# Performance work log

Measured on AMD Instinct MI355X. Metric: run time of the kernel, lower is better.

The kernel has to match this reference:

```python
import jax, jax.numpy as jnp
import numpy as np
from jax import lax

L, CB, D, K = 4, 256, 512, 3   # layers, bottleneck, dconv_size, kernel
B, T = 16, 4096                # batch, frames
EPS = 1e-5


def _binarize(w):
    # bitwise weight quantization: sign(w), straight-through in bwd
    return w + lax.stop_gradient(jnp.sign(w) - w)


def _conv1d(x, w, b, dilation=1, groups=1, pad=(0, 0)):
    # x: [N, C, T], w: [O, I/groups, K]
    y = lax.conv_general_dilated(
        x, w, window_strides=(1,), padding=[pad], rhs_dilation=(dilation,),
        dimension_numbers=("NCH", "OIH", "NCH"), feature_group_count=groups)
    return y + b[None, :, None]


def _prelu(x, a):
    return jnp.where(x >= 0, x, a * x)


def _bn(x, g, b):
    # training-mode BatchNorm1d over (batch, time) per channel
    mean = jnp.mean(x, axis=(0, 2), keepdims=True)
    var = jnp.var(x, axis=(0, 2), keepdims=True)
    xn = (x - mean) * lax.rsqrt(var + EPS)
    return xn * g[None, :, None] + b[None, :, None]


def setup_inputs() -> dict:
    key = jax.random.key(0)
    ks = jax.random.split(key, 8)
    s = 0.05
    return {
        "x":   jax.random.normal(ks[0], (B, CB, T), jnp.float32),
        "w1":  jax.random.normal(ks[1], (L, D, CB, 1), jnp.float32) * s,
        "b1":  jnp.zeros((L, D), jnp.float32),
        "a1":  jnp.full((L,), 0.25, jnp.float32),
        "g1":  jnp.ones((L, D), jnp.float32),
        "be1": jnp.zeros((L, D), jnp.float32),
        "wd":  jax.random.normal(ks[2], (L, D, 1, K), jnp.float32) * s,
        "bd":  jnp.zeros((L, D), jnp.float32),
        "a2":  jnp.full((L,), 0.25, jnp.float32),
        "g2":  jnp.ones((L, D), jnp.float32),
        "be2": jnp.zeros((L, D), jnp.float32),
        "w2":  jax.random.normal(ks[3], (L, CB, D, 1), jnp.float32) * s,
        "b2":  jnp.zeros((L, CB), jnp.float32),
    }


def reference(x, w1, b1, a1, g1, be1, wd, bd, a2, g2, be2, w2, b2):
    resid = x
    for i in range(L):
        dil = 2 ** i
        pad_left = dil * (K - 1)  # causal/chomped padding keeps length T
        x = _conv1d(x, _binarize(w1[i]), b1[i])                       # 1x1: CB->D
        x = _bn(_prelu(x, a1[i]), g1[i], be1[i])
        x = _conv1d(x, _binarize(wd[i]), bd[i], dilation=dil,
                    groups=D, pad=(pad_left, 0))                       # depthwise dilated
        x = _bn(_prelu(x, a2[i]), g2[i], be2[i])
        x = _conv1d(x, _binarize(w2[i]), b2[i])                       # 1x1: D->CB
    return x + resid
```

## Files before the change

kernel.cpp:

```cpp
#include <hip/hip_runtime.h>
#include <stdint.h>
#include <stddef.h>

#define NL   4
#define CBC  256
#define DCH  512
#define KW   3
#define BATCH 16
#define TT   4096
#define BT   (BATCH*TT)
#define EPSB 1e-5f

typedef __bf16 bf16_t;
typedef __attribute__((ext_vector_type(8))) __bf16 bf16x8;
typedef __attribute__((ext_vector_type(4))) float f32x4;
typedef __attribute__((ext_vector_type(8))) unsigned short us8;
typedef __attribute__((ext_vector_type(4))) unsigned short us4;

static __device__ __forceinline__ unsigned short f2bf(float f) {
    union { float f; uint32_t u; } v; v.f = f;
    uint32_t u = v.u;
    u += 0x7FFFu + ((u >> 16) & 1u);
    return (unsigned short)(u >> 16);
}
static __device__ __forceinline__ float bf2f(unsigned short b) {
    union { uint32_t u; float f; } v; v.u = ((uint32_t)b) << 16;
    return v.f;
}
static __device__ __forceinline__ bf16x8 as_bf16x8(us8 u) {
    return __builtin_bit_cast(bf16x8, u);
}
static __device__ __forceinline__ float signf_(float w) {
    return (w > 0.f) ? 1.f : ((w < 0.f) ? -1.f : 0.f);
}

typedef __attribute__((address_space(1))) void as1_void;
typedef __attribute__((address_space(3))) void as3_void;
static __device__ __forceinline__ void gload_lds16(const unsigned short* g, unsigned short* l) {
    __builtin_amdgcn_global_load_lds((as1_void*)g, (as3_void*)l, 16, 0, 0);
}

__global__ void prep_kernel(const float* __restrict__ w1, const float* __restrict__ wd,
                            unsigned short* __restrict__ W1S, float* __restrict__ WDS) {
    const int NW1 = NL * DCH * CBC;
    const int NWD = NL * DCH * KW;
    int idx = blockIdx.x * 256 + threadIdx.x;
    if (idx < NW1) {
        W1S[idx] = f2bf(signf_(w1[idx]));
    } else if (idx < NW1 + NWD) {
        int j = idx - NW1;
        WDS[j] = signf_(wd[j]);
    }
}

__global__ void transpose_in(const float* __restrict__ x, unsigned short* __restrict__ XA) {
    __shared__ unsigned short tile[64][72];
    const int t0 = blockIdx.x * 64, c0 = blockIdx.y * 64, b = blockIdx.z;
    const int tid = threadIdx.x;
    {
        const int cl = tid >> 2;
        const int tl = (tid & 3) * 16;
        const float* src = x + ((size_t)(b * CBC + c0 + cl)) * TT + t0 + tl;
        #pragma unroll
        for (int u = 0; u < 16; u += 4) {
            float4 f = *(const float4*)(src + u);
            tile[cl][tl + u + 0] = f2bf(f.x);
            tile[cl][tl + u + 1] = f2bf(f.y);
            tile[cl][tl + u + 2] = f2bf(f.z);
            tile[cl][tl + u + 3] = f2bf(f.w);
        }
    }
    __syncthreads();
    {
        const int tr = tid >> 2;
        const int cc = (tid & 3) * 16;
        us8 o0, o1;
        #pragma unroll
        for (int e = 0; e < 8; ++e) { o0[e] = tile[cc + e][tr]; o1[e] = tile[cc + 8 + e][tr]; }
        unsigned short* dst = XA + ((size_t)(b * TT + t0 + tr)) * CBC + c0 + cc;
        *(us8*)dst = o0;
        *(us8*)(dst + 8) = o1;
    }
}

template<int K, int NMT, bool PRELU, bool FINAL, bool STATS>
__global__ __launch_bounds__(256, 4)
void gemm_kernel(const unsigned short* __restrict__ A,
                 const unsigned short* __restrict__ Bact,
                 const float* __restrict__ bias,
                 const float* __restrict__ aptr,
                 unsigned short* __restrict__ Obf,
                 float* __restrict__ Ofin,
                 const float* __restrict__ resid,
                 float* __restrict__ sums, float* __restrict__ sqs,
                 int M) {
    __shared__ union {
        unsigned short stage[2][4][2048];
        unsigned short sout[128 * 136];
    } sm;
    __shared__ float sstat[2][4][64];

    const int tid = threadIdx.x;

    const int nwg = NMT * (TT / 128) * BATCH;
    const int orig = blockIdx.x;
    const int logical = (orig & 7) * (nwg >> 3) + (orig >> 3);
    const int mt = logical % NMT;
    const int rest = logical / NMT;
    const int tt = rest & 31;
    const int bz = rest >> 5;
    const int t0 = tt * 128;
    const int m0 = mt * 128;
    const size_t n0 = (size_t)bz * TT + t0;

    const int lane = tid & 63;
    const int w    = tid >> 6;
    const int wm = w & 1, wn = w >> 1;
    const int l16 = lane & 15, q = lane >> 4;

    const int rS = tid >> 2;
    const int cS = ((tid & 3) ^ ((tid >> 3) & 3)) * 8;
    const unsigned short* gA0 = A + (size_t)(m0 + rS) * K + cS;
    const unsigned short* gA1 = A + (size_t)(m0 + 64 + rS) * K + cS;
    const unsigned short* gB0 = Bact + (n0 + rS) * K + cS;
    const unsigned short* gB1 = Bact + (n0 + 64 + rS) * K + cS;
    const int wofs = w << 9;

    auto STAGE = [&](int step, int buf) {
        const int k0 = step * 32;
        unsigned short* sb = &sm.stage[buf][0][0];
        gload_lds16(gA0 + k0, sb + 0 * 2048 + wofs);
        gload_lds16(gA1 + k0, sb + 1 * 2048 + wofs);
        gload_lds16(gB0 + k0, sb + 2 * 2048 + wofs);
        gload_lds16(gB1 + k0, sb + 3 * 2048 + wofs);
    };

    f32x4 acc[4][4];
    #pragma unroll
    for (int i = 0; i < 4; ++i)
        #pragma unroll
        for (int j = 0; j < 4; ++j)
            acc[i][j] = (f32x4){0.f, 0.f, 0.f, 0.f};

    const int csw = (q ^ ((l16 >> 1) & 3)) << 3;

    constexpr int NK = K / 32;
    STAGE(0, 0);
    asm volatile("s_waitcnt vmcnt(0)" ::: "memory");
    __builtin_amdgcn_s_barrier();
    __builtin_amdgcn_sched_barrier(0);

    #pragma unroll
    for (int k = 0; k < NK; ++k) {
        const int cur = k & 1;
        if (k + 1 < NK) STAGE(k + 1, cur ^ 1);
        const unsigned short* sb = &sm.stage[cur][0][0];
        bf16x8 af[4], bfv[4];
        #pragma unroll
        for (int i = 0; i < 4; ++i)
            af[i] = as_bf16x8(*(const us8*)(sb + wm * 2048 + (i * 16 + l16) * 32 + csw));
        #pragma unroll
        for (int j = 0; j < 4; ++j)
            bfv[j] = as_bf16x8(*(const us8*)(sb + (2 + wn) * 2048 + (j * 16 + l16) * 32 + csw));
        #pragma unroll
        for (int i = 0; i < 4; ++i)
            #pragma unroll
            for (int j = 0; j < 4; ++j)
                acc[i][j] = __builtin_amdgcn_mfma_f32_16x16x32_bf16(af[i], bfv[j], acc[i][j], 0, 0, 0);
        if (k + 1 < NK) {
            asm volatile("s_waitcnt vmcnt(0)" ::: "memory");
            __builtin_amdgcn_sched_barrier(0);
        }
        __builtin_amdgcn_s_barrier();
        __builtin_amdgcn_sched_barrier(0);
    }

    float alpha = 0.f;
    if constexpr (PRELU) alpha = aptr[0];

    if constexpr (FINAL) {
        #pragma unroll
        for (int i = 0; i < 4; ++i) {
            const int m_l = wm * 64 + i * 16 + q * 4;
            float bia[4];
            #pragma unroll
            for (int rg = 0; rg < 4; ++rg) bia[rg] = bias[m0 + m_l + rg];
            #pragma unroll
            for (int j = 0; j < 4; ++j) {
                const int n_l = wn * 64 + j * 16 + l16;
                const int t = t0 + n_l;
                #pragma unroll
                for (int rg = 0; rg < 4; ++rg) {
                    float v = acc[i][j][rg] + bia[rg];
                    size_t oidx = ((size_t)(bz * CBC + m0 + m_l + rg)) * TT + t;
                    Ofin[oidx] = v + resid[oidx];
                }
            }
        }
    } else {
        #pragma unroll
        for (int i = 0; i < 4; ++i) {
            const int m_l = wm * 64 + i * 16 + q * 4;
            float bia[4];
            #pragma unroll
            for (int rg = 0; rg < 4; ++rg) bia[rg] = bias[m0 + m_l + rg];
            #pragma unroll
            for (int j = 0; j < 4; ++j) {
                const int n_l = wn * 64 + j * 16 + l16;
                us4 pkv;
                #pragma unroll
                for (int rg = 0; rg < 4; ++rg) {
                    float v = acc[i][j][rg] + bia[rg];
                    if (PRELU) v = (v >= 0.f) ? v : alpha * v;
                    pkv[rg] = f2bf(v);
                }
                *(us4*)&sm.sout[n_l * 136 + m_l] = pkv;
            }
            if constexpr (STATS) {
                #pragma unroll
                for (int rg = 0; rg < 4; ++rg) {
                    float sv = 0.f, sq2 = 0.f;
                    #pragma unroll
                    for (int j = 0; j < 4; ++j) {
                        float v = acc[i][j][rg] + bia[rg];
                        if (PRELU) v = (v >= 0.f) ? v : alpha * v;
                        sv += v; sq2 += v * v;
                    }
                    #pragma unroll
                    for (int msk = 1; msk < 16; msk <<= 1) {
                        sv  += __shfl_xor(sv,  msk, 64);
                        sq2 += __shfl_xor(sq2, msk, 64);
                    }
                    if (l16 == 0) {
                        const int cl = i * 16 + q * 4 + rg;
                        sstat[0][w][cl] = sv;
                        sstat[1][w][cl] = sq2;
                    }
                }
            }
        }
        __syncthreads();
        const int rr = tid >> 4;
        const int c8 = (tid & 15) * 8;
        #pragma unroll
        for (int p = 0; p < 8; ++p) {
            const int n_l = p * 16 + rr;
            us8 v = *(const us8*)&sm.sout[n_l * 136 + c8];
            *(us8*)(Obf + (n0 + n_l) * M + m0 + c8) = v;
        }
        if constexpr (STATS) {
            if (tid < 128) {
                const int wmc = tid >> 6, cl = tid & 63;
                float S = sstat[0][wmc][cl] + sstat[0][wmc + 2][cl];
                float Q = sstat[1][wmc][cl] + sstat[1][wmc + 2][cl];
                atomicAdd(&sums[m0 + tid], S);
                atomicAdd(&sqs[m0 + tid], Q);
            }
        }
    }
}

__global__ __launch_bounds__(256)
void dwconv_kernel(const unsigned short* __restrict__ Y,
                   const float* __restrict__ sums1, const float* __restrict__ sqs1,
                   const float* __restrict__ g1, const float* __restrict__ be1,
                   const float* __restrict__ wds, const float* __restrict__ bd,
                   const float* __restrict__ a2p, int dil,
                   unsigned short* __restrict__ Z,
                   float* __restrict__ sums2, float* __restrict__ sqs2) {
    __shared__ float ssum[4][256];
    __shared__ float ssq[4][256];
    const int b = blockIdx.z;
    const int half = blockIdx.y;
    const int t0 = blockIdx.x * 64;
    const int tid = threadIdx.x;
    const int w = tid >> 6;
    const int lane = tid & 63;
    const int r = lane >> 5;
    const int cl = (lane & 31) * 8;
    const int c0 = half * 256 + cl;
    const float alpha = a2p[0];

    float s8[8], sh8[8], wv0[8], wv1[8], wv2[8], bb8[8];
    const float inv = 1.f / (float)BT;
    #pragma unroll
    for (int e = 0; e < 8; ++e) {
        const int d = c0 + e;
        float mean = sums1[d] * inv;
        float var = sqs1[d] * inv - mean * mean;
        float sc = g1[d] * rsqrtf(var + EPSB);
        s8[e] = sc;
        sh8[e] = be1[d] - mean * sc;
        wv0[e] = wds[d * 3 + 0]; wv1[e] = wds[d * 3 + 1]; wv2[e] = wds[d * 3 + 2];
        bb8[e] = bd[d];
    }

    float asum[8], asq[8];
    #pragma unroll
    for (int e = 0; e < 8; ++e) { asum[e] = 0.f; asq[e] = 0.f; }

    if (blockIdx.x == 0) {
        for (int it = 0; it < 8; ++it) {
            const int t = it * 8 + 2 * w + r;
            const size_t base = ((size_t)b * TT + t) * DCH + c0;
            float acc[8];
            {
                us8 y0 = *(const us8*)&Y[base];
                #pragma unroll
                for (int e = 0; e < 8; ++e)
                    acc[e] = wv2[e] * (s8[e] * bf2f(y0[e]) + sh8[e]) + bb8[e];
            }
            if (t >= dil) {
                us8 y1 = *(const us8*)&Y[base - (size_t)dil * DCH];
                #pragma unroll
                for (int e = 0; e < 8; ++e)
                    acc[e] += wv1[e] * (s8[e] * bf2f(y1[e]) + sh8[e]);
            }
            if (t >= 2 * dil) {
                us8 y2 = *(const us8*)&Y[base - (size_t)(2 * dil) * DCH];
                #pragma unroll
                for (int e = 0; e < 8; ++e)
                    acc[e] += wv0[e] * (s8[e] * bf2f(y2[e]) + sh8[e]);
            }
            us8 o;
            #pragma unroll
            for (int e = 0; e < 8; ++e) {
                float v = acc[e];
                v = (v >= 0.f) ? v : alpha * v;
                asum[e] += v; asq[e] += v * v;
                o[e] = f2bf(v);
            }
            *(us8*)&Z[base] = o;
        }
    } else {
        float W0s[8], W1s[8], W2s[8], shall[8];
        #pragma unroll
        for (int e = 0; e < 8; ++e) {
            W0s[e] = wv0[e] * s8[e];
            W1s[e] = wv1[e] * s8[e];
            W2s[e] = wv2[e] * s8[e];
            shall[e] = (wv0[e] + wv1[e] + wv2[e]) * sh8[e] + bb8[e];
        }
        const size_t d1 = (size_t)dil * DCH, d2 = 2 * d1;
        for (int it = 0; it < 8; ++it) {
            const int t = t0 + it * 8 + 2 * w + r;
            const size_t base = ((size_t)b * TT + t) * DCH + c0;
            us8 y0 = *(const us8*)&Y[base];
            us8 y1 = *(const us8*)&Y[base - d1];
            us8 y2 = *(const us8*)&Y[base - d2];
            us8 o;
            #pragma unroll
            for (int e = 0; e < 8; ++e) {
                float v = W2s[e] * bf2f(y0[e]) + W1s[e] * bf2f(y1[e])
                        + W0s[e] * bf2f(y2[e]) + shall[e];
                v = (v >= 0.f) ? v : alpha * v;
                asum[e] += v; asq[e] += v * v;
                o[e] = f2bf(v);
            }
            *(us8*)&Z[base] = o;
        }
    }

    #pragma unroll
    for (int e = 0; e < 8; ++e) {
        asum[e] += __shfl_xor(asum[e], 32, 64);
        asq[e]  += __shfl_xor(asq[e], 32, 64);
    }
    if (lane < 32) {
        #pragma unroll
        for (int e = 0; e < 8; ++e) { ssum[w][cl + e] = asum[e]; ssq[w][cl + e] = asq[e]; }
    }
    __syncthreads();
    {
        const int ch = tid;
        float S = ssum[0][ch] + ssum[1][ch] + ssum[2][ch] + ssum[3][ch];
        float Q = ssq[0][ch] + ssq[1][ch] + ssq[2][ch] + ssq[3][ch];
        atomicAdd(&sums2[half * 256 + ch], S);
        atomicAdd(&sqs2[half * 256 + ch], Q);
    }
}

__global__ void fold_kernel(const float* __restrict__ w2,
                            const float* __restrict__ sums2, const float* __restrict__ sqs2,
                            const float* __restrict__ g2, const float* __restrict__ be2,
                            const float* __restrict__ b2,
                            unsigned short* __restrict__ W2E, float* __restrict__ B2E) {
    __shared__ float red[256];
    const int c = blockIdx.x, tid = threadIdx.x;
    const float inv = 1.f / (float)BT;
    float part = 0.f;
    for (int d = tid; d < DCH; d += 256) {
        float mean = sums2[d] * inv;
        float var = sqs2[d] * inv - mean * mean;
        float sc = g2[d] * rsqrtf(var + EPSB);
        float shf = be2[d] - mean * sc;
        float w = w2[(size_t)c * DCH + d];
        float sgn = signf_(w);
        W2E[(size_t)c * DCH + d] = f2bf(sgn * sc);
        part += sgn * shf;
    }
    red[tid] = part;
    __syncthreads();
    for (int off = 128; off > 0; off >>= 1) {
        if (tid < off) red[tid] += red[tid + off];
        __syncthreads();
    }
    if (tid == 0) B2E[c] = b2[c] + red[0];
}

extern "C" void kernel_launch(void* const* d_in, const int* in_sizes, int n_in,
                              void* d_out, int out_size, void* d_ws, size_t ws_size,
                              hipStream_t stream) {
    const float* x   = (const float*)d_in[0];
    const float* w1  = (const float*)d_in[1];
    const float* b1  = (const float*)d_in[2];
    const float* a1  = (const float*)d_in[3];
    const float* g1  = (const float*)d_in[4];
    const float* be1 = (const float*)d_in[5];
    const float* wd  = (const float*)d_in[6];
    const float* bd  = (const float*)d_in[7];
    const float* a2  = (const float*)d_in[8];
    const float* g2  = (const float*)d_in[9];
    const float* be2 = (const float*)d_in[10];
    const float* w2  = (const float*)d_in[11];
    const float* b2  = (const float*)d_in[12];
    float* out = (float*)d_out;

    char* ws = (char*)d_ws;
    size_t off = 0;
    auto alloc = [&](size_t bytes) -> void* {
        void* p = ws + off;
        off += (bytes + 255) & ~(size_t)255;
        return p;
    };
    unsigned short* XA  = (unsigned short*)alloc((size_t)BT * CBC * 2);
    unsigned short* Y   = (unsigned short*)alloc((size_t)BT * DCH * 2);
    unsigned short* Z   = (unsigned short*)alloc((size_t)BT * DCH * 2);
    unsigned short* W1S = (unsigned short*)alloc((size_t)NL * DCH * CBC * 2);
    float* WDS          = (float*)alloc((size_t)NL * DCH * KW * 4);
    unsigned short* W2E = (unsigned short*)alloc((size_t)CBC * DCH * 2);
    float* B2E          = (float*)alloc((size_t)CBC * 4);
    float* stats = (float*)alloc((size_t)4 * NL * 512 * 4);
    float* sums1 = stats + 0 * NL * 512;
    float* sqs1  = stats + 1 * NL * 512;
    float* sums2 = stats + 2 * NL * 512;
    float* sqs2  = stats + 3 * NL * 512;

    (void)hipMemsetAsync(stats, 0, (size_t)4 * NL * 512 * 4, stream);

    {
        const int NTOT = NL * DCH * CBC + NL * DCH * KW;
        prep_kernel<<<(NTOT + 255) / 256, 256, 0, stream>>>(w1, wd, W1S, WDS);
    }
    transpose_in<<<dim3(TT / 64, CBC / 64, BATCH), 256, 0, stream>>>(x, XA);

    const int NWG1 = (DCH / 128) * (TT / 128) * BATCH;
    const int NWG2 = (CBC / 128) * (TT / 128) * BATCH;

    for (int l = 0; l < NL; ++l) {
        gemm_kernel<CBC, DCH / 128, true, false, true><<<NWG1, 256, 0, stream>>>(
            W1S + (size_t)l * DCH * CBC, XA, b1 + (size_t)l * DCH, a1 + l,
            Y, nullptr, nullptr, sums1 + l * 512, sqs1 + l * 512, DCH);
        dwconv_kernel<<<dim3(TT / 64, 2, BATCH), 256, 0, stream>>>(
            Y, sums1 + l * 512, sqs1 + l * 512, g1 + (size_t)l * DCH, be1 + (size_t)l * DCH,
            WDS + (size_t)l * DCH * KW, bd + (size_t)l * DCH, a2 + l, 1 << l,
            Z, sums2 + l * 512, sqs2 + l * 512);
        fold_kernel<<<CBC, 256, 0, stream>>>(w2 + (size_t)l * CBC * DCH,
                                             sums2 + l * 512, sqs2 + l * 512,
                                             g2 + (size_t)l * DCH, be2 + (size_t)l * DCH,
                                             b2 + (size_t)l * CBC, W2E, B2E);
        if (l < NL - 1) {
            gemm_kernel<DCH, CBC / 128, false, false, false><<<NWG2, 256, 0, stream>>>(
                W2E, Z, B2E, nullptr, XA, nullptr, nullptr, nullptr, nullptr, CBC);
        } else {
            gemm_kernel<DCH, CBC / 128, false, true, false><<<NWG2, 256, 0, stream>>>(
                W2E, Z, B2E, nullptr, nullptr, out, x, nullptr, nullptr, CBC);
        }
    }
}
```

Measured before the change: 580.5 us.

## Widen GEMM block tile to 128x256 with 8 waves sharing the A tile

The 1x1-conv GEMM kernel now uses 512 threads (8 waves) per block and covers 256 time frames instead of 128. The weight (A) tile is staged once per K step and shared by twice as many columns, which cuts LDS staging traffic and global weight loads per output. The epilogue writes the bf16 output through shared memory in two halves with extra barriers, and the stats reduction now sums over 8 waves. The costs are half as many blocks, a larger LDS footprint and more barrier synchronisation in the epilogue.

```diff
diff --git a/kernel.cpp b/kernel.cpp
--- a/kernel.cpp
+++ b/kernel.cpp
@@ -84,7 +84,7 @@
 }
 
 template<int K, int NMT, bool PRELU, bool FINAL, bool STATS>
-__global__ __launch_bounds__(256, 4)
+__global__ __launch_bounds__(512, 6)
 void gemm_kernel(const unsigned short* __restrict__ A,
                  const unsigned short* __restrict__ Bact,
                  const float* __restrict__ bias,
@@ -95,21 +95,21 @@
                  float* __restrict__ sums, float* __restrict__ sqs,
                  int M) {
     __shared__ union {
-        unsigned short stage[2][4][2048];
+        unsigned short stage[2][12288];
         unsigned short sout[128 * 136];
     } sm;
-    __shared__ float sstat[2][4][64];
+    __shared__ float sstat[2][8][64];
 
     const int tid = threadIdx.x;
 
-    const int nwg = NMT * (TT / 128) * BATCH;
+    const int nwg = NMT * (TT / 256) * BATCH;
     const int orig = blockIdx.x;
     const int logical = (orig & 7) * (nwg >> 3) + (orig >> 3);
     const int mt = logical % NMT;
     const int rest = logical / NMT;
-    const int tt = rest & 31;
-    const int bz = rest >> 5;
-    const int t0 = tt * 128;
+    const int tt = rest & 15;
+    const int bz = rest >> 4;
+    const int t0 = tt * 256;
     const int m0 = mt * 128;
     const size_t n0 = (size_t)bz * TT + t0;
 
@@ -120,19 +120,17 @@
 
     const int rS = tid >> 2;
     const int cS = ((tid & 3) ^ ((tid >> 3) & 3)) * 8;
-    const unsigned short* gA0 = A + (size_t)(m0 + rS) * K + cS;
-    const unsigned short* gA1 = A + (size_t)(m0 + 64 + rS) * K + cS;
+    const unsigned short* gA  = A + (size_t)(m0 + rS) * K + cS;
     const unsigned short* gB0 = Bact + (n0 + rS) * K + cS;
-    const unsigned short* gB1 = Bact + (n0 + 64 + rS) * K + cS;
+    const unsigned short* gB1 = Bact + (n0 + 128 + rS) * K + cS;
     const int wofs = w << 9;
 
     auto STAGE = [&](int step, int buf) {
         const int k0 = step * 32;
-        unsigned short* sb = &sm.stage[buf][0][0];
-        gload_lds16(gA0 + k0, sb + 0 * 2048 + wofs);
-        gload_lds16(gA1 + k0, sb + 1 * 2048 + wofs);
-        gload_lds16(gB0 + k0, sb + 2 * 2048 + wofs);
-        gload_lds16(gB1 + k0, sb + 3 * 2048 + wofs);
+        unsigned short* sb = &sm.stage[buf][0];
+        gload_lds16(gA  + k0, sb + wofs);
+        gload_lds16(gB0 + k0, sb + 4096 + wofs);
+        gload_lds16(gB1 + k0, sb + 8192 + wofs);
     };
 
     f32x4 acc[4][4];
@@ -154,14 +152,14 @@
     for (int k = 0; k < NK; ++k) {
         const int cur = k & 1;
         if (k + 1 < NK) STAGE(k + 1, cur ^ 1);
-        const unsigned short* sb = &sm.stage[cur][0][0];
+        const unsigned short* sb = &sm.stage[cur][0];
         bf16x8 af[4], bfv[4];
         #pragma unroll
         for (int i = 0; i < 4; ++i)
-            af[i] = as_bf16x8(*(const us8*)(sb + wm * 2048 + (i * 16 + l16) * 32 + csw));
+            af[i] = as_bf16x8(*(const us8*)(sb + (wm * 64 + i * 16 + l16) * 32 + csw));
         #pragma unroll
         for (int j = 0; j < 4; ++j)
-            bfv[j] = as_bf16x8(*(const us8*)(sb + (2 + wn) * 2048 + (j * 16 + l16) * 32 + csw));
+            bfv[j] = as_bf16x8(*(const us8*)(sb + 4096 + (wn * 64 + j * 16 + l16) * 32 + csw));
         #pragma unroll
         for (int i = 0; i < 4; ++i)
             #pragma unroll
@@ -198,25 +196,13 @@
             }
         }
     } else {
-        #pragma unroll
-        for (int i = 0; i < 4; ++i) {
-            const int m_l = wm * 64 + i * 16 + q * 4;
-            float bia[4];
-            #pragma unroll
-            for (int rg = 0; rg < 4; ++rg) bia[rg] = bias[m0 + m_l + rg];
-            #pragma unroll
-            for (int j = 0; j < 4; ++j) {
-                const int n_l = wn * 64 + j * 16 + l16;
-                us4 pkv;
-                #pragma unroll
-                for (int rg = 0; rg < 4; ++rg) {
-                    float v = acc[i][j][rg] + bia[rg];
-                    if (PRELU) v = (v >= 0.f) ? v : alpha * v;
-                    pkv[rg] = f2bf(v);
-                }
-                *(us4*)&sm.sout[n_l * 136 + m_l] = pkv;
-            }
-            if constexpr (STATS) {
+        if constexpr (STATS) {
+            #pragma unroll
+            for (int i = 0; i < 4; ++i) {
+                const int m_l = wm * 64 + i * 16 + q * 4;
+                float bia[4];
+                #pragma unroll
+                for (int rg = 0; rg < 4; ++rg) bia[rg] = bias[m0 + m_l + rg];
                 #pragma unroll
                 for (int rg = 0; rg < 4; ++rg) {
                     float sv = 0.f, sq2 = 0.f;
@@ -239,20 +225,51 @@
                 }
             }
         }
-        __syncthreads();
-        const int rr = tid >> 4;
-        const int c8 = (tid & 15) * 8;
-        #pragma unroll
-        for (int p = 0; p < 8; ++p) {
-            const int n_l = p * 16 + rr;
-            us8 v = *(const us8*)&sm.sout[n_l * 136 + c8];
-            *(us8*)(Obf + (n0 + n_l) * M + m0 + c8) = v;
+        #pragma unroll
+        for (int p = 0; p < 2; ++p) {
+            if ((wn >> 1) == p) {
+                #pragma unroll
+                for (int i = 0; i < 4; ++i) {
+                    const int m_l = wm * 64 + i * 16 + q * 4;
+                    float bia[4];
+                    #pragma unroll
+                    for (int rg = 0; rg < 4; ++rg) bia[rg] = bias[m0 + m_l + rg];
+                    #pragma unroll
+                    for (int j = 0; j < 4; ++j) {
+                        const int n_l = (wn & 1) * 64 + j * 16 + l16;
+                        us4 pkv;
+                        #pragma unroll
+                        for (int rg = 0; rg < 4; ++rg) {
+                            float v = acc[i][j][rg] + bia[rg];
+                            if (PRELU) v = (v >= 0.f) ? v : alpha * v;
+                            pkv[rg] = f2bf(v);
+                        }
+                        *(us4*)&sm.sout[n_l * 136 + m_l] = pkv;
+                    }
+                }
+            }
+            __syncthreads();
+            {
+                const int rr = tid >> 4;
+                const int c8 = (tid & 15) * 8;
+                #pragma unroll
+                for (int pp = 0; pp < 4; ++pp) {
+                    const int n_l = pp * 32 + rr;
+                    us8 v = *(const us8*)&sm.sout[n_l * 136 + c8];
+                    *(us8*)(Obf + (n0 + p * 128 + n_l) * M + m0 + c8) = v;
+                }
+            }
+            __syncthreads();
         }
         if constexpr (STATS) {
             if (tid < 128) {
                 const int wmc = tid >> 6, cl = tid & 63;
-                float S = sstat[0][wmc][cl] + sstat[0][wmc + 2][cl];
-                float Q = sstat[1][wmc][cl] + sstat[1][wmc + 2][cl];
+                float S = 0.f, Q = 0.f;
+                #pragma unroll
+                for (int wq = 0; wq < 4; ++wq) {
+                    S += sstat[0][wq * 2 + wmc][cl];
+                    Q += sstat[1][wq * 2 + wmc][cl];
+                }
                 atomicAdd(&sums[m0 + tid], S);
                 atomicAdd(&sqs[m0 + tid], Q);
             }
@@ -454,11 +471,11 @@
     }
     transpose_in<<<dim3(TT / 64, CBC / 64, BATCH), 256, 0, stream>>>(x, XA);
 
-    const int NWG1 = (DCH / 128) * (TT / 128) * BATCH;
-    const int NWG2 = (CBC / 128) * (TT / 128) * BATCH;
+    const int NWG1 = (DCH / 128) * (TT / 256) * BATCH;
+    const int NWG2 = (CBC / 128) * (TT / 256) * BATCH;
 
     for (int l = 0; l < NL; ++l) {
-        gemm_kernel<CBC, DCH / 128, true, false, true><<<NWG1, 256, 0, stream>>>(
+        gemm_kernel<CBC, DCH / 128, true, false, true><<<NWG1, 512, 0, stream>>>(
             W1S + (size_t)l * DCH * CBC, XA, b1 + (size_t)l * DCH, a1 + l,
             Y, nullptr, nullptr, sums1 + l * 512, sqs1 + l * 512, DCH);
         dwconv_kernel<<<dim3(TT / 64, 2, BATCH), 256, 0, stream>>>(
@@ -470,10 +487,10 @@
                                              g2 + (size_t)l * DCH, be2 + (size_t)l * DCH,
                                              b2 + (size_t)l * CBC, W2E, B2E);
         if (l < NL - 1) {
-            gemm_kernel<DCH, CBC / 128, false, false, false><<<NWG2, 256, 0, stream>>>(
+            gemm_kernel<DCH, CBC / 128, false, false, false><<<NWG2, 512, 0, stream>>>(
                 W2E, Z, B2E, nullptr, XA, nullptr, nullptr, nullptr, nullptr, CBC);
         } else {
-            gemm_kernel<DCH, CBC / 128, false, true, false><<<NWG2, 256, 0, stream>>>(
+            gemm_kernel<DCH, CBC / 128, false, true, false><<<NWG2, 512, 0, stream>>>(
                 W2E, Z, B2E, nullptr, nullptr, out, x, nullptr, nullptr, CBC);
         }
     }
```

Result: slower. 1.329 ms (+128.9%).
